# Optimization experiments

Hardware: AMD Instinct MI355X
Metric: run time of the kernel (lower is better)

Reference implementation:

```python
import jax, jax.numpy as jnp
import numpy as np

B, T, D_IN, D_OUT = 4, 2048, 1024, 1024


def setup_inputs() -> dict:
    key = jax.random.key(0)
    k1, k2, k3, k4 = jax.random.split(key, 4)
    x = jax.random.normal(k1, (B, T, D_IN), dtype=jnp.float32)
    W_q = jax.random.normal(k2, (D_OUT, D_IN), dtype=jnp.float32) * 0.02
    W_k = jax.random.normal(k3, (D_OUT, D_IN), dtype=jnp.float32) * 0.02
    W_v = jax.random.normal(k4, (D_OUT, D_IN), dtype=jnp.float32) * 0.02
    return {"x": x, "W_q": W_q, "W_k": W_k, "W_v": W_v}


def reference(x, W_q, W_k, W_v):
    b, t, d_in = x.shape
    d_out = W_q.shape[0]
    # Linear projections (torch Linear: y = x @ W.T), no bias
    q = jnp.einsum("btd,od->bto", x, W_q)
    k = jnp.einsum("btd,od->bto", x, W_k)
    v = jnp.einsum("btd,od->bto", x, W_v)
    # Raw scores [b, t, t]
    scores = jnp.einsum("bqd,bkd->bqk", q, k)
    # Faithful to the source: tril with diagonal=1 => position i sees j <= i+1
    mask = jnp.tril(jnp.ones((t, t), dtype=bool), k=1)
    scores = jnp.where(mask, scores, -jnp.inf)
    # Scale by sqrt(d_out) (full d_out, single head), stable softmax
    attn = jax.nn.softmax(scores / jnp.sqrt(jnp.asarray(d_out, x.dtype)), axis=-1)
    # dropout=0.0 -> identity
    return jnp.einsum("bqk,bkd->bqd", attn, v)
```

## Files before the change

kernel.cpp:

```cpp
#include <hip/hip_runtime.h>
#include <hip/hip_bf16.h>

typedef unsigned short u16;
typedef __attribute__((ext_vector_type(8))) short short8v;
typedef __attribute__((ext_vector_type(4))) float float4v;

__device__ inline u16 f2b(float f) {
  __hip_bfloat16 h = __float2bfloat16(f);
  union { __hip_bfloat16 h; u16 s; } u;
  u.h = h;
  return u.s;
}

__device__ inline float b2f(u16 s) {
  union { u16 s[2]; float f; } u;
  u.s[0] = 0; u.s[1] = s;
  return u.f;
}

__device__ inline void gload_lds16(const u16* g, u16* l) {
  __builtin_amdgcn_global_load_lds(
      (const __attribute__((address_space(1))) void*)g,
      (__attribute__((address_space(3))) void*)l, 16, 0, 0);
}

__global__ __launch_bounds__(256) void cvt_f32_bf16(const float* __restrict__ in,
                                                    u16* __restrict__ out, int n4) {
  for (int i = blockIdx.x * blockDim.x + threadIdx.x; i < n4;
       i += gridDim.x * blockDim.x) {
    float4 v = ((const float4*)in)[i];
    ushort4 o;
    o.x = f2b(v.x); o.y = f2b(v.y); o.z = f2b(v.z); o.w = f2b(v.w);
    ((ushort4*)out)[i] = o;
  }
}

__global__ __launch_bounds__(256)
void cvt_w3(const float* __restrict__ wa, const float* __restrict__ wb,
            const float* __restrict__ wc, u16* __restrict__ oa,
            u16* __restrict__ ob, u16* __restrict__ oc, int n4each) {
  int i = blockIdx.x * blockDim.x + threadIdx.x;
  const float* src; u16* dst; int off;
  if (i < n4each)            { src = wa; dst = oa; off = i; }
  else if (i < 2 * n4each)   { src = wb; dst = ob; off = i - n4each; }
  else                       { src = wc; dst = oc; off = i - 2 * n4each; }
  float4 v = ((const float4*)src)[off];
  ushort4 o;
  o.x = f2b(v.x); o.y = f2b(v.y); o.z = f2b(v.z); o.w = f2b(v.w);
  ((ushort4*)dst)[off] = o;
}

template <int MODE, typename CT>
__global__ __launch_bounds__(256, 2)
void gemm8(const u16* __restrict__ A, int lda, long sA,
           const u16* __restrict__ B, int ldb, long sB,
           CT* __restrict__ C, int ldc, long sC, int K) {
  constexpr int BM = 128, BN = 128;
  constexpr int A_U16 = BM * 64;
  constexpr int TILE_U16 = (BM + BN) * 64;
  constexpr int TILE_BYTES = TILE_U16 * 2;
  __shared__ __align__(16) u16 lds[2 * TILE_U16];

  const int z = blockIdx.z;
  A += (long)z * sA;
  B += (long)z * sB;

  int bx = blockIdx.x;
  if (MODE == 2) bx = gridDim.x - 1 - bx;
  const int m0 = bx * BM;
  const int n0 = blockIdx.y * BN;
  if (MODE == 1 && n0 > m0 + BM) return;
  int Keff = K;
  if (MODE == 2) Keff = min(m0 + BM + 1, K);
  const int nk = (Keff + 63) >> 6;

  const int tid  = threadIdx.x;
  const int lane = tid & 63;
  const int wid  = tid >> 6;
  const int wr   = wid >> 1;
  const int wc   = wid & 1;

  const u16* gsrc[8];
  int loff[8];
#pragma unroll
  for (int j = 0; j < 4; ++j) {
    int c = tid + j * 256;
    int r = c >> 3;
    int kg = ((c & 7) ^ (r & 7)) * 8;
    gsrc[j] = A + (long)(m0 + r) * lda + kg;
    loff[j] = c * 8;
  }
#pragma unroll
  for (int j = 0; j < 4; ++j) {
    int c = tid + j * 256;
    int r = c >> 3;
    int kg = ((c & 7) ^ (r & 7)) * 8;
    gsrc[4 + j] = B + (long)(n0 + r) * ldb + kg;
    loff[4 + j] = A_U16 + c * 8;
  }

#define STAGE_ALL(T_, DST_)                                                 \
  {                                                                         \
    _Pragma("unroll")                                                       \
    for (int s = 0; s < 8; ++s)                                             \
      gload_lds16(gsrc[s] + (long)(T_) * 64, (DST_) + loff[s]);             \
  }

  const int kl  = (lane >> 4) * 16;
  const int swz = (lane & 7) << 4;
  const int kx0 = kl ^ swz;
  const int kx1 = (64 + kl) ^ swz;
  const int abase = (wr * 64 + (lane & 15)) * 128;
  const int bbase = 2 * A_U16 + (wc * 64 + (lane & 15)) * 128;

  float4v acc[4][4];
#pragma unroll
  for (int i = 0; i < 4; ++i)
#pragma unroll
    for (int j = 0; j < 4; ++j)
      acc[i][j] = (float4v){0.f, 0.f, 0.f, 0.f};

  STAGE_ALL(0, lds);
  asm volatile("s_waitcnt vmcnt(0)" ::: "memory");
  __builtin_amdgcn_s_barrier();

  for (int t = 0; t < nk; ++t) {
    const char* bb = (const char*)lds + (t & 1) * TILE_BYTES;
    u16* sb = lds + ((t & 1) ^ 1) * TILE_U16;

    if (t + 1 < nk) STAGE_ALL(t + 1, sb);

    short8v a0[4], b0[4], a1[4], b1[4];
#pragma unroll
    for (int mi = 0; mi < 4; ++mi)
      a0[mi] = *(const short8v*)(bb + abase + mi * 2048 + kx0);
#pragma unroll
    for (int ni = 0; ni < 4; ++ni)
      b0[ni] = *(const short8v*)(bb + bbase + ni * 2048 + kx0);
    __builtin_amdgcn_sched_barrier(0);
#pragma unroll
    for (int mi = 0; mi < 4; ++mi)
      a1[mi] = *(const short8v*)(bb + abase + mi * 2048 + kx1);
#pragma unroll
    for (int ni = 0; ni < 4; ++ni)
      b1[ni] = *(const short8v*)(bb + bbase + ni * 2048 + kx1);

    asm volatile("s_waitcnt lgkmcnt(8)" ::: "memory");
    __builtin_amdgcn_sched_barrier(0);
    __builtin_amdgcn_s_setprio(1);
#pragma unroll
    for (int mi = 0; mi < 4; ++mi)
#pragma unroll
      for (int ni = 0; ni < 4; ++ni)
        acc[mi][ni] = __builtin_amdgcn_mfma_f32_16x16x32_bf16(
            a0[mi], b0[ni], acc[mi][ni], 0, 0, 0);
    __builtin_amdgcn_s_setprio(0);

    asm volatile("s_waitcnt lgkmcnt(0)" ::: "memory");
    __builtin_amdgcn_sched_barrier(0);
    __builtin_amdgcn_s_setprio(1);
#pragma unroll
    for (int mi = 0; mi < 4; ++mi)
#pragma unroll
      for (int ni = 0; ni < 4; ++ni)
        acc[mi][ni] = __builtin_amdgcn_mfma_f32_16x16x32_bf16(
            a1[mi], b1[ni], acc[mi][ni], 0, 0, 0);
    __builtin_amdgcn_s_setprio(0);

    asm volatile("s_waitcnt vmcnt(0)" ::: "memory");
    __builtin_amdgcn_s_barrier();
  }
#undef STAGE_ALL

  CT* c = C + (long)z * sC;
  const int r0base = m0 + wr * 64 + ((lane >> 4) << 2);
  const int cbase  = n0 + wc * 64 + (lane & 15);
#pragma unroll
  for (int mi = 0; mi < 4; ++mi) {
#pragma unroll
    for (int ni = 0; ni < 4; ++ni) {
      const int r0 = r0base + mi * 16;
      const int cc = cbase + ni * 16;
#pragma unroll
      for (int r = 0; r < 4; ++r) {
        float v = acc[mi][ni][r];
        if constexpr (__is_same(CT, float)) c[(long)(r0 + r) * ldc + cc] = v;
        else                                c[(long)(r0 + r) * ldc + cc] = f2b(v);
      }
    }
  }
}

__global__ __launch_bounds__(256)
void softmax_kernel(u16* __restrict__ SP, int T) {
  const int  i    = blockIdx.x & (T - 1);
  const long base = (long)blockIdx.x * T;
  const int  nvis = min(i + 2, T);
  const int  capJ = min(T, ((i >> 7) << 7) + 192);
  const float scale = 0.03125f;

  __shared__ float red[4];

  const int j0 = threadIdx.x * 8;
  float v[8];
  float m = -INFINITY;
  if (j0 < nvis) {
    short8v raw = *(const short8v*)&SP[base + j0];
#pragma unroll
    for (int e = 0; e < 8; ++e) {
      float f = (j0 + e < nvis) ? b2f((u16)raw[e]) * scale : -INFINITY;
      v[e] = f;
      m = fmaxf(m, f);
    }
  }
#pragma unroll
  for (int o = 32; o; o >>= 1) m = fmaxf(m, __shfl_xor(m, o));
  const int wid = threadIdx.x >> 6;
  if ((threadIdx.x & 63) == 0) red[wid] = m;
  __syncthreads();
  m = fmaxf(fmaxf(red[0], red[1]), fmaxf(red[2], red[3]));
  __syncthreads();

  float s = 0.f;
  if (j0 < nvis) {
#pragma unroll
    for (int e = 0; e < 8; ++e) {
      float p = (j0 + e < nvis) ? __expf(v[e] - m) : 0.f;
      v[e] = p;
      s += p;
    }
  }
#pragma unroll
  for (int o = 32; o; o >>= 1) s += __shfl_xor(s, o);
  if ((threadIdx.x & 63) == 0) red[wid] = s;
  __syncthreads();
  s = red[0] + red[1] + red[2] + red[3];
  const float inv = 1.0f / s;

  if (j0 < capJ) {
    short8v o8;
#pragma unroll
    for (int e = 0; e < 8; ++e)
      o8[e] = (short)f2b((j0 + e < nvis) ? v[e] * inv : 0.f);
    *(short8v*)&SP[base + j0] = o8;
  }
}

extern "C" void kernel_launch(void* const* d_in, const int* in_sizes, int n_in,
                              void* d_out, int out_size, void* d_ws, size_t ws_size,
                              hipStream_t stream) {
  const float* x  = (const float*)d_in[0];
  const float* Wq = (const float*)d_in[1];
  const float* Wk = (const float*)d_in[2];
  const float* Wv = (const float*)d_in[3];
  float* out = (float*)d_out;

  const int B = 4, T = 2048, D = 1024;
  const int M = B * T;
  const long TT = (long)T * T;

  char* ws = (char*)d_ws;
  u16* qk  = (u16*)(ws);
  u16* vt  = (u16*)(ws + (32l << 20));
  u16* xb  = (u16*)(ws + (48l << 20));
  u16* wqk = (u16*)(ws + (64l << 20));
  u16* wv  = (u16*)(ws + (68l << 20));
  u16* S   = (u16*)(ws + (48l << 20));

  cvt_f32_bf16<<<2048, 256, 0, stream>>>(x, xb, (M * D) / 4);
  cvt_w3<<<3 * (D * D / 4) / 256, 256, 0, stream>>>(
      Wq, Wk, Wv, wqk, wqk + (long)D * D, wv, D * D / 4);

  gemm8<0, u16><<<dim3(M / 128, 2 * D / 128, 1), 256, 0, stream>>>(
      xb, D, 0, wqk, D, 0, qk, 2 * D, 0, D);
  gemm8<0, u16><<<dim3(D / 128, M / 128, 1), 256, 0, stream>>>(
      wv, D, 0, xb, D, 0, vt, M, 0, D);

  gemm8<1, u16><<<dim3(T / 128, T / 128, B), 256, 0, stream>>>(
      qk, 2 * D, (long)T * 2 * D,
      qk + D, 2 * D, (long)T * 2 * D,
      S, T, TT, D);

  softmax_kernel<<<B * T, 256, 0, stream>>>(S, T);

  gemm8<2, float><<<dim3(T / 128, D / 128, B), 256, 0, stream>>>(
      S, T, TT,
      vt, M, T,
      out, D, (long)T * D, T);
}
```

Measured before the change: 161.8 us.

## Add 256x256-tile 8-wave GEMM with phased LDS pipeline for QK projection and scores

Adds a new GEMM kernel with 256x256 output tiles, 512 threads and a 128 KB double-buffered LDS, split into half-K stages. Global-to-LDS loads are interleaved with MFMA phases under explicit barriers, waitcnt and setprio scheduling. It is used for the fused Q/K projection and the causal score GEMM, which skips fully masked tiles at the coarser granularity. The larger tiles raise arithmetic intensity and cut global traffic, at the cost of one block per CU, high register pressure and coarser causal skipping.

```diff
diff --git a/kernel.cpp b/kernel.cpp
--- a/kernel.cpp
+++ b/kernel.cpp
@@ -51,6 +51,131 @@
 }
 
 template <int MODE, typename CT>
+__global__ __launch_bounds__(512, 1)
+void gemm9(const u16* __restrict__ A, int lda, long sA,
+           const u16* __restrict__ B, int ldb, long sB,
+           CT* __restrict__ C, int ldc, long sC, int K) {
+  __shared__ __align__(16) u16 lds[65536];
+
+  const int z = blockIdx.z;
+  A += (long)z * sA;
+  B += (long)z * sB;
+
+  const int m0 = blockIdx.x * 256;
+  const int n0 = blockIdx.y * 256;
+  if (MODE == 1 && n0 > m0 + 256) return;
+  const int nk = K >> 6;
+
+  const int tid  = threadIdx.x;
+  const int lane = tid & 63;
+  const int wid  = tid >> 6;
+  const int wr   = wid >> 2;
+  const int wc   = wid & 3;
+
+  const u16* gA[2]; const u16* gB[2]; int lof[2];
+#pragma unroll
+  for (int j = 0; j < 2; ++j) {
+    int c = tid + j * 512;
+    int r = c >> 2;
+    int l = (c & 3) ^ ((r >> 1) & 3);
+    gA[j] = A + (long)(m0 + r) * lda + l * 8;
+    gB[j] = B + (long)(n0 + r) * ldb + l * 8;
+    lof[j] = c * 8;
+  }
+
+#define STAGE_U(T_, KH_, MAT_, D_)                                          \
+  {                                                                         \
+    u16* dst_ = lds + (D_) * 32768 + ((MAT_) * 2 + (KH_)) * 8192;           \
+    _Pragma("unroll")                                                       \
+    for (int j = 0; j < 2; ++j)                                             \
+      gload_lds16(((MAT_) ? gB[j] : gA[j]) + (long)(T_) * 64 + (KH_) * 32,  \
+                  dst_ + lof[j]);                                           \
+  }
+
+  const int swzt = 16 * ((lane >> 4) ^ ((lane >> 1) & 3));
+  const int aoff = (wr * 128 + (lane & 15)) * 64 + swzt;
+  const int boff = (wc * 64 + (lane & 15)) * 64 + swzt;
+  const char* ldsc = (const char*)lds;
+
+  float4v acc[8][4];
+#pragma unroll
+  for (int i = 0; i < 8; ++i)
+#pragma unroll
+    for (int j = 0; j < 4; ++j)
+      acc[i][j] = (float4v){0.f, 0.f, 0.f, 0.f};
+
+  short8v b_[4];
+
+#define PHASE(D_, KS_, MH_, READB_, STAGE_STMT_, VM_)                       \
+  {                                                                         \
+    const char* ab_ = ldsc + (D_) * 65536 + (KS_) * 16384;                  \
+    const char* bb_ = ldsc + (D_) * 65536 + 32768 + (KS_) * 16384;          \
+    short8v a_[4];                                                          \
+    _Pragma("unroll")                                                       \
+    for (int mi = 0; mi < 4; ++mi)                                          \
+      a_[mi] = *(const short8v*)(ab_ + aoff + (MH_) * 4096 + mi * 1024);    \
+    if (READB_) {                                                           \
+      _Pragma("unroll")                                                     \
+      for (int ni = 0; ni < 4; ++ni)                                        \
+        b_[ni] = *(const short8v*)(bb_ + boff + ni * 1024);                 \
+    }                                                                       \
+    STAGE_STMT_;                                                            \
+    __builtin_amdgcn_s_barrier();                                           \
+    asm volatile("s_waitcnt lgkmcnt(0)" ::: "memory");                      \
+    __builtin_amdgcn_sched_barrier(0);                                      \
+    __builtin_amdgcn_s_setprio(1);                                          \
+    _Pragma("unroll")                                                       \
+    for (int mi = 0; mi < 4; ++mi)                                          \
+      _Pragma("unroll")                                                     \
+      for (int ni = 0; ni < 4; ++ni)                                        \
+        acc[(MH_) * 4 + mi][ni] = __builtin_amdgcn_mfma_f32_16x16x32_bf16(  \
+            a_[mi], b_[ni], acc[(MH_) * 4 + mi][ni], 0, 0, 0);              \
+    __builtin_amdgcn_s_setprio(0);                                          \
+    if (VM_) asm volatile("s_waitcnt vmcnt(4)" ::: "memory");               \
+    __builtin_amdgcn_s_barrier();                                           \
+  }
+
+  STAGE_U(0, 0, 0, 0); STAGE_U(0, 0, 1, 0);
+  STAGE_U(0, 1, 0, 0); STAGE_U(0, 1, 1, 0);
+  STAGE_U(1, 0, 0, 1); STAGE_U(1, 0, 1, 1);
+  asm volatile("s_waitcnt vmcnt(4)" ::: "memory");
+  __builtin_amdgcn_s_barrier();
+
+  for (int it = 0; it < (nk >> 1); ++it) {
+    const int t0 = 2 * it, t1 = 2 * it + 1;
+    const bool s2 = (t0 + 2 < nk), s3 = (t1 + 2 < nk);
+    PHASE(0, 0, 0, true,  { STAGE_U(t1, 1, 0, 1); },           false);
+    PHASE(0, 0, 1, false, { STAGE_U(t1, 1, 1, 1); },           false);
+    PHASE(0, 1, 0, true,  { if (s2) STAGE_U(t0 + 2, 0, 0, 0); }, false);
+    PHASE(0, 1, 1, false, { if (s2) STAGE_U(t0 + 2, 0, 1, 0); }, true);
+    PHASE(1, 0, 0, true,  { if (s2) STAGE_U(t0 + 2, 1, 0, 0); }, false);
+    PHASE(1, 0, 1, false, { if (s2) STAGE_U(t0 + 2, 1, 1, 0); }, false);
+    PHASE(1, 1, 0, true,  { if (s3) STAGE_U(t1 + 2, 0, 0, 1); }, false);
+    PHASE(1, 1, 1, false, { if (s3) STAGE_U(t1 + 2, 0, 1, 1); }, true);
+  }
+#undef PHASE
+#undef STAGE_U
+
+  CT* c = C + (long)z * sC;
+  const int r0base = m0 + wr * 128 + ((lane >> 4) << 2);
+  const int cbase  = n0 + wc * 64 + (lane & 15);
+#pragma unroll
+  for (int mi = 0; mi < 8; ++mi) {
+#pragma unroll
+    for (int ni = 0; ni < 4; ++ni) {
+      const int r0 = r0base + mi * 16;
+      const int cc = cbase + ni * 16;
+#pragma unroll
+      for (int r = 0; r < 4; ++r) {
+        float v = acc[mi][ni][r];
+        if constexpr (__is_same(CT, float)) c[(long)(r0 + r) * ldc + cc] = v;
+        else                                c[(long)(r0 + r) * ldc + cc] = f2b(v);
+      }
+    }
+  }
+}
+
+template <int MODE, typename CT>
 __global__ __launch_bounds__(256, 2)
 void gemm8(const u16* __restrict__ A, int lda, long sA,
            const u16* __restrict__ B, int ldb, long sB,
@@ -271,12 +396,12 @@
   cvt_w3<<<3 * (D * D / 4) / 256, 256, 0, stream>>>(
       Wq, Wk, Wv, wqk, wqk + (long)D * D, wv, D * D / 4);
 
-  gemm8<0, u16><<<dim3(M / 128, 2 * D / 128, 1), 256, 0, stream>>>(
+  gemm9<0, u16><<<dim3(M / 256, 2 * D / 256, 1), 512, 0, stream>>>(
       xb, D, 0, wqk, D, 0, qk, 2 * D, 0, D);
   gemm8<0, u16><<<dim3(D / 128, M / 128, 1), 256, 0, stream>>>(
       wv, D, 0, xb, D, 0, vt, M, 0, D);
 
-  gemm8<1, u16><<<dim3(T / 128, T / 128, B), 256, 0, stream>>>(
+  gemm9<1, u16><<<dim3(T / 256, T / 256, B), 512, 0, stream>>>(
       qk, 2 * D, (long)T * 2 * D,
       qk + D, 2 * D, (long)T * 2 * D,
       S, T, TT, D);
```

Measured after the change: 166.2 us. 1.03x slower.

## Merge V projection and QK^T score GEMMs into one launch

Applied to the files above, without the earlier changes.

Moves the GEMM body into a shared device function and adds a combined kernel whose first 512 blocks compute the V-transpose projection while the remaining blocks compute the causal QK^T score tiles. S is relocated so it no longer overlaps xb, which the V projection still reads in the same launch. This removes one kernel launch and lets the two independent GEMMs fill the device together instead of each leaving a partly occupied tail. The PV GEMM also reverses its block order only for the first two batches, which changes its scheduling. Early-returning masked blocks still use grid slots.

```diff
diff --git a/kernel.cpp b/kernel.cpp
--- a/kernel.cpp
+++ b/kernel.cpp
@@ -50,29 +50,15 @@
   ((ushort4*)dst)[off] = o;
 }
 
-template <int MODE, typename CT>
-__global__ __launch_bounds__(256, 2)
-void gemm8(const u16* __restrict__ A, int lda, long sA,
-           const u16* __restrict__ B, int ldb, long sB,
-           CT* __restrict__ C, int ldc, long sC, int K) {
-  constexpr int BM = 128, BN = 128;
-  constexpr int A_U16 = BM * 64;
-  constexpr int TILE_U16 = (BM + BN) * 64;
-  constexpr int TILE_BYTES = TILE_U16 * 2;
+template <typename CT>
+__device__ __forceinline__ void gemm_core(
+    const u16* __restrict__ A, int lda,
+    const u16* __restrict__ B, int ldb,
+    CT* __restrict__ C, int ldc, int m0, int n0, int nk) {
+  constexpr int A_U16 = 8192;
+  constexpr int TILE_U16 = 16384;
+  constexpr int TILE_BYTES = 32768;
   __shared__ __align__(16) u16 lds[2 * TILE_U16];
-
-  const int z = blockIdx.z;
-  A += (long)z * sA;
-  B += (long)z * sB;
-
-  int bx = blockIdx.x;
-  if (MODE == 2) bx = gridDim.x - 1 - bx;
-  const int m0 = bx * BM;
-  const int n0 = blockIdx.y * BN;
-  if (MODE == 1 && n0 > m0 + BM) return;
-  int Keff = K;
-  if (MODE == 2) Keff = min(m0 + BM + 1, K);
-  const int nk = (Keff + 63) >> 6;
 
   const int tid  = threadIdx.x;
   const int lane = tid & 63;
@@ -172,7 +158,6 @@
   }
 #undef STAGE_ALL
 
-  CT* c = C + (long)z * sC;
   const int r0base = m0 + wr * 64 + ((lane >> 4) << 2);
   const int cbase  = n0 + wc * 64 + (lane & 15);
 #pragma unroll
@@ -184,11 +169,48 @@
 #pragma unroll
       for (int r = 0; r < 4; ++r) {
         float v = acc[mi][ni][r];
-        if constexpr (__is_same(CT, float)) c[(long)(r0 + r) * ldc + cc] = v;
-        else                                c[(long)(r0 + r) * ldc + cc] = f2b(v);
+        if constexpr (__is_same(CT, float)) C[(long)(r0 + r) * ldc + cc] = v;
+        else                                C[(long)(r0 + r) * ldc + cc] = f2b(v);
       }
     }
   }
+}
+
+template <int MODE, typename CT>
+__global__ __launch_bounds__(256, 2)
+void gemm8(const u16* __restrict__ A, int lda, long sA,
+           const u16* __restrict__ B, int ldb, long sB,
+           CT* __restrict__ C, int ldc, long sC, int K) {
+  const int z = blockIdx.z;
+  int bx = blockIdx.x;
+  if (MODE == 2 && z < 2) bx = gridDim.x - 1 - bx;
+  const int m0 = bx * 128;
+  const int n0 = blockIdx.y * 128;
+  int Keff = K;
+  if (MODE == 2) Keff = min(m0 + 129, K);
+  gemm_core<CT>(A + (long)z * sA, lda, B + (long)z * sB, ldb,
+                C + (long)z * sC, ldc, m0, n0, (Keff + 63) >> 6);
+}
+
+__global__ __launch_bounds__(256, 2)
+void gemm_vts(const u16* __restrict__ xb, const u16* __restrict__ wv,
+              const u16* __restrict__ qk, u16* __restrict__ vt,
+              u16* __restrict__ S) {
+  const int bid = blockIdx.x;
+  const u16 *A, *B; u16* C; int lda, ldc, m0, n0;
+  if (bid < 512) {
+    A = wv; B = xb; C = vt; lda = 1024; ldc = 8192;
+    m0 = (bid & 7) * 128; n0 = (bid >> 3) * 128;
+  } else {
+    const int sid = bid - 512;
+    const int z = sid >> 8, r = sid & 255;
+    m0 = (r & 15) * 128; n0 = (r >> 4) * 128;
+    if (n0 > m0 + 128) return;
+    const long zo = (long)z * 4194304;
+    A = qk + zo; B = qk + zo + 1024; C = S + zo;
+    lda = 2048; ldc = 2048;
+  }
+  gemm_core<u16>(A, lda, B, lda, C, ldc, m0, n0, 16);
 }
 
 __global__ __launch_bounds__(256)
@@ -265,7 +287,7 @@
   u16* xb  = (u16*)(ws + (48l << 20));
   u16* wqk = (u16*)(ws + (64l << 20));
   u16* wv  = (u16*)(ws + (68l << 20));
-  u16* S   = (u16*)(ws + (48l << 20));
+  u16* S   = (u16*)(ws + (72l << 20));
 
   cvt_f32_bf16<<<2048, 256, 0, stream>>>(x, xb, (M * D) / 4);
   cvt_w3<<<3 * (D * D / 4) / 256, 256, 0, stream>>>(
@@ -273,13 +295,8 @@
 
   gemm8<0, u16><<<dim3(M / 128, 2 * D / 128, 1), 256, 0, stream>>>(
       xb, D, 0, wqk, D, 0, qk, 2 * D, 0, D);
-  gemm8<0, u16><<<dim3(D / 128, M / 128, 1), 256, 0, stream>>>(
-      wv, D, 0, xb, D, 0, vt, M, 0, D);
-
-  gemm8<1, u16><<<dim3(T / 128, T / 128, B), 256, 0, stream>>>(
-      qk, 2 * D, (long)T * 2 * D,
-      qk + D, 2 * D, (long)T * 2 * D,
-      S, T, TT, D);
+
+  gemm_vts<<<512 + 1024, 256, 0, stream>>>(xb, wv, qk, vt, S);
 
   softmax_kernel<<<B * T, 256, 0, stream>>>(S, T);
 
```

After: 152.9 us. 1.06x faster.
